# Performance work log

Hardware: AMD Instinct MI355X
Metric: run time of the kernel (lower is better)

Reference implementation:

```python
import jax, jax.numpy as jnp
import numpy as np


def setup_inputs() -> dict:
    key = jax.random.key(0)
    k1, k2, k3, k4 = jax.random.split(key, 4)
    N, F, E = 100000, 128, 1600000
    Fo = F // 2
    x = jax.random.normal(k1, (N, F), dtype=jnp.float32)
    edge_index = jax.random.randint(k2, (2, E), 0, N, dtype=jnp.int32)
    W_conv = jax.random.normal(k3, (Fo, F), dtype=jnp.float32) * (1.0 / np.sqrt(F))
    b_conv = jnp.zeros((Fo,), dtype=jnp.float32)
    W_lin = jax.random.normal(k4, (1, Fo), dtype=jnp.float32) * (1.0 / np.sqrt(Fo))
    b_lin = jnp.zeros((1,), dtype=jnp.float32)
    return {"x": x, "edge_index": edge_index, "W_conv": W_conv,
            "b_conv": b_conv, "W_lin": W_lin, "b_lin": b_lin}


def gcn_conv(x, edge_index, W_conv, b_conv):
    # PyG GCNConv: add self-loops, symmetric normalization, x@W.T, scatter-add, + bias
    N = x.shape[0]
    loops = jnp.arange(N, dtype=edge_index.dtype)
    src = jnp.concatenate([edge_index[0], loops])  # message sources
    dst = jnp.concatenate([edge_index[1], loops])  # aggregation targets
    h = x @ W_conv.T  # [N, Fo]
    deg = jax.ops.segment_sum(jnp.ones_like(dst, dtype=h.dtype), dst, num_segments=N)
    dinv = jnp.where(deg > 0, jax.lax.rsqrt(deg), 0.0)
    norm = dinv[src] * dinv[dst]  # [E+N]
    msg = h[src] * norm[:, None]  # [E+N, Fo] -- dominant memory traffic
    agg = jax.ops.segment_sum(msg, dst, num_segments=N)
    return agg + b_conv


def reference(x, edge_index, W_conv, b_conv, W_lin, b_lin):
    h = gcn_conv(x, edge_index, W_conv, b_conv)
    h = jax.nn.relu(h)
    logits = h @ W_lin.T + b_lin  # [N, 1]
    return jax.nn.sigmoid(logits)
```

## Files before the change

kernel.cpp:

```cpp
#include <hip/hip_runtime.h>
#include <hip/hip_bf16.h>
#include <math.h>

#define F_IN   128
#define F_OUT  64
#define CHUNK  5120
#define MAXB   512
#define PADSLACK 4096

typedef short bf16x8 __attribute__((ext_vector_type(8)));
typedef float f32x4  __attribute__((ext_vector_type(4)));

__device__ __forceinline__ float bf2f(unsigned short u) {
    union { unsigned int i; float f; } c; c.i = ((unsigned int)u) << 16; return c.f;
}
__device__ __forceinline__ unsigned short f2bf(float f) {
    union { float f; unsigned int i; } c; c.f = f;
    unsigned int r = c.i + 0x7FFFu + ((c.i >> 16) & 1u);
    return (unsigned short)(r >> 16);
}
__device__ __forceinline__ unsigned int pk2bf(float a, float b) {
    __hip_bfloat162 p = __float22bfloat162_rn(make_float2(a, b));
    union { __hip_bfloat162 h; unsigned int u; } c; c.h = p; return c.u;
}
__device__ __forceinline__ float u_lo(unsigned int u) {
    union { unsigned int i; float f; } c; c.i = u << 16; return c.f;
}
__device__ __forceinline__ float u_hi(unsigned int u) {
    union { unsigned int i; float f; } c; c.i = u & 0xFFFF0000u; return c.f;
}

__global__ __launch_bounds__(256) void k_hist(
    const int* __restrict__ dst, int E, int* __restrict__ M, int NBLK, int NBC) {
    __shared__ int hist[MAXB];
    for (int c = threadIdx.x; c < MAXB; c += 256) hist[c] = 0;
    __syncthreads();
    int e0 = blockIdx.x * CHUNK;
    int e1 = min(E, e0 + CHUNK);
    for (int e = e0 + threadIdx.x; e < e1; e += 256)
        atomicAdd(&hist[dst[e] >> 8], 1);
    __syncthreads();
    for (int c = threadIdx.x; c < NBC; c += 256)
        M[c * NBLK + blockIdx.x] = hist[c];
}

__global__ void k_scan1(const int* __restrict__ M, int* __restrict__ tmp,
                        int* __restrict__ bsum, int S) {
    __shared__ int sh[256];
    int i = blockIdx.x * 256 + threadIdx.x;
    int v = (i < S) ? M[i] : 0;
    sh[threadIdx.x] = v;
    __syncthreads();
    for (int off = 1; off < 256; off <<= 1) {
        int t = (threadIdx.x >= off) ? sh[threadIdx.x - off] : 0;
        __syncthreads();
        sh[threadIdx.x] += t;
        __syncthreads();
    }
    if (i < S) tmp[i] = sh[threadIdx.x];
    if (threadIdx.x == 255) bsum[blockIdx.x] = sh[255];
}

__global__ void k_scan2(int* __restrict__ bsum, int NB1) {
    __shared__ int sh[512];
    int v = (threadIdx.x < NB1) ? bsum[threadIdx.x] : 0;
    sh[threadIdx.x] = v;
    __syncthreads();
    for (int off = 1; off < 512; off <<= 1) {
        int t = (threadIdx.x >= off) ? sh[threadIdx.x - off] : 0;
        __syncthreads();
        sh[threadIdx.x] += t;
        __syncthreads();
    }
    if (threadIdx.x < NB1) bsum[threadIdx.x] = sh[threadIdx.x] - v;
}

__global__ void k_scan3(int* __restrict__ M, const int* __restrict__ tmp,
                        const int* __restrict__ bsum, int* __restrict__ bucketOff,
                        int S, int NBLK, int NBC, int E) {
    int i = blockIdx.x * 256 + threadIdx.x;
    if (i < S) {
        int orig = M[i];
        int o = tmp[i] - orig + bsum[blockIdx.x];
        M[i] = o;
        if (i % NBLK == 0) bucketOff[i / NBLK] = o;
    }
    if (i == 0) bucketOff[NBC] = E;
}

__global__ __launch_bounds__(256) void k_scatter(
    const int* __restrict__ src, const int* __restrict__ dst, int E,
    const int* __restrict__ M, int NBLK, int NBC, unsigned int* __restrict__ entries) {
    __shared__ int cur[MAXB];
    for (int c = threadIdx.x; c < NBC; c += 256)
        cur[c] = M[c * NBLK + blockIdx.x];
    __syncthreads();
    int e0 = blockIdx.x * CHUNK;
    int e1 = min(E, e0 + CHUNK);
    for (int e = e0 + threadIdx.x; e < e1; e += 256) {
        int d = dst[e];
        int s = src[e];
        int p = atomicAdd(&cur[d >> 8], 1);
        entries[p] = ((unsigned int)(d & 255) << 24) | (unsigned int)s;
    }
}

__global__ __launch_bounds__(256) void k_sort(
    const unsigned int* __restrict__ entries, const int* __restrict__ bucketOff,
    int* __restrict__ offsetsP, int* __restrict__ deg,
    unsigned int* __restrict__ srcsP, int N) {
    __shared__ int hist[256];
    __shared__ int curs[256];
    const int tid = threadIdx.x;
    const int b = blockIdx.x;
    const int start = bucketOff[b];
    const int end   = bucketOff[b + 1];
    const int startP = start + b * PADSLACK;

    hist[tid] = 0;
    __syncthreads();
    for (int i = start + tid; i < end; i += 256)
        atomicAdd(&hist[entries[i] >> 24], 1);
    __syncthreads();

    int cntv   = hist[tid];
    int padded = (cntv + 15) & ~15;
    curs[tid] = padded;
    __syncthreads();
    for (int off = 1; off < 256; off <<= 1) {
        int t = (tid >= off) ? curs[tid - off] : 0;
        __syncthreads();
        curs[tid] += t;
        __syncthreads();
    }
    int exclP = curs[tid] - padded;
    int d = (b << 8) + tid;
    if (d < N) { offsetsP[d] = startP + exclP; deg[d] = cntv; }
    __syncthreads();
    curs[tid] = startP + exclP;
    __syncthreads();

    for (int i = start + tid; i < end; i += 256) {
        unsigned int v = entries[i];
        int p = atomicAdd(&curs[v >> 24], 1);
        srcsP[p] = (v & 0xFFFFFFu) << 7;
    }
    __syncthreads();

    int padEnd = startP + exclP + padded;
    unsigned int sent = ((unsigned int)N) << 7;
    for (int p = curs[tid]; p < padEnd; ++p)
        srcsP[p] = sent;
}

__global__ __launch_bounds__(256) void k_gemm(
    const float* __restrict__ x, const float* __restrict__ W,
    const int* __restrict__ deg, unsigned short* __restrict__ g, int N) {
    __shared__ unsigned short xs[64 * F_IN];
    __shared__ unsigned short Wsh[F_OUT * F_IN];
    __shared__ float dinvs[64];

    const int tid  = threadIdx.x;
    const int row0 = blockIdx.x * 64;

    {
        const float4* W4 = (const float4*)W;
        #pragma unroll
        for (int t = 0; t < 8; ++t) {
            int idx = t * 256 + tid;
            float4 v = W4[idx];
            uint2 u = make_uint2(pk2bf(v.x, v.y), pk2bf(v.z, v.w));
            *(uint2*)&Wsh[idx * 4] = u;
        }
    }
    {
        const float4* x4 = (const float4*)x;
        #pragma unroll
        for (int t = 0; t < 8; ++t) {
            int idx = t * 256 + tid;
            int r = idx >> 5;
            int grow = row0 + r;
            float4 v = make_float4(0.f, 0.f, 0.f, 0.f);
            if (grow < N) v = x4[(size_t)grow * 32 + (idx & 31)];
            uint2 u = make_uint2(pk2bf(v.x, v.y), pk2bf(v.z, v.w));
            *(uint2*)&xs[idx * 4] = u;
        }
    }
    if (tid < 64) {
        int grow = row0 + tid;
        float dv = 1.0f;
        if (grow < N) dv = rsqrtf((float)deg[grow] + 1.0f);
        dinvs[tid] = dv;
    }
    __syncthreads();

    const int lane = tid & 63;
    const int wave = tid >> 6;
    const int m = lane & 15;
    const int q = lane >> 4;
    const int r0 = wave * 16;

    bf16x8 a[4];
    #pragma unroll
    for (int ks = 0; ks < 4; ++ks)
        a[ks] = *(const bf16x8*)&xs[(r0 + m) * F_IN + ks * 32 + q * 8];

    f32x4 acc[4] = {{0,0,0,0},{0,0,0,0},{0,0,0,0},{0,0,0,0}};
    #pragma unroll
    for (int ct = 0; ct < 4; ++ct) {
        #pragma unroll
        for (int ks = 0; ks < 4; ++ks) {
            bf16x8 b = *(const bf16x8*)&Wsh[(ct * 16 + m) * F_IN + ks * 32 + q * 8];
            acc[ct] = __builtin_amdgcn_mfma_f32_16x16x32_bf16(a[ks], b, acc[ct], 0, 0, 0);
        }
    }

    float dv[4];
    #pragma unroll
    for (int reg = 0; reg < 4; ++reg)
        dv[reg] = dinvs[r0 + q * 4 + reg];
    #pragma unroll
    for (int ct = 0; ct < 4; ++ct) {
        #pragma unroll
        for (int reg = 0; reg < 4; ++reg) {
            int grow = row0 + r0 + q * 4 + reg;
            if (grow <= N)
                g[(size_t)grow * F_OUT + ct * 16 + m] = f2bf(acc[ct][reg] * dv[reg]);
        }
    }
}

__global__ __launch_bounds__(256) void k_pull(
    const unsigned short* __restrict__ g, const int* __restrict__ offsetsP,
    const int* __restrict__ deg, const unsigned int* __restrict__ srcsP,
    const float* __restrict__ b_conv, const float* __restrict__ W_lin,
    const float* __restrict__ b_lin, float* __restrict__ out, int N) {
    const int lane   = threadIdx.x & 63;
    const int grp    = lane >> 3;
    const int s      = lane & 7;
    const int wave   = (blockIdx.x * blockDim.x + threadIdx.x) >> 6;
    const int nwaves = (gridDim.x * blockDim.x) >> 6;

    const float2* b2 = (const float2*)b_conv;
    const float2* w2 = (const float2*)W_lin;
    float2 bb[4], wl[4];
    #pragma unroll
    for (int j = 0; j < 4; ++j) { bb[j] = b2[s * 4 + j]; wl[j] = w2[s * 4 + j]; }
    const float bl = b_lin[0];
    const float selfm = (grp == 0) ? 1.0f : 0.0f;

    const char* gb = (const char*)g;
    const unsigned int seg = ((unsigned int)s) << 4;

    for (int i = wave; i < N; i += nwaves) {
        int e0 = __builtin_amdgcn_readfirstlane(offsetsP[i]);
        int dg = __builtin_amdgcn_readfirstlane(deg[i]);
        int niter = (dg + 15) >> 4;

        uint4 us = *(const uint4*)(gb + (size_t)(((unsigned int)i << 7) | seg));
        float2 acc[4];
        acc[0] = make_float2(selfm * u_lo(us.x), selfm * u_hi(us.x));
        acc[1] = make_float2(selfm * u_lo(us.y), selfm * u_hi(us.y));
        acc[2] = make_float2(selfm * u_lo(us.z), selfm * u_hi(us.z));
        acc[3] = make_float2(selfm * u_lo(us.w), selfm * u_hi(us.w));

        const unsigned int* sp = srcsP + e0;
        for (int it = 0; it < niter; ++it) {
            unsigned int o0 = sp[grp];
            unsigned int o1 = sp[8 + grp];
            uint4 uA = *(const uint4*)(gb + (size_t)(o0 | seg));
            uint4 uB = *(const uint4*)(gb + (size_t)(o1 | seg));
            acc[0].x += u_lo(uA.x); acc[0].y += u_hi(uA.x);
            acc[1].x += u_lo(uA.y); acc[1].y += u_hi(uA.y);
            acc[2].x += u_lo(uA.z); acc[2].y += u_hi(uA.z);
            acc[3].x += u_lo(uA.w); acc[3].y += u_hi(uA.w);
            acc[0].x += u_lo(uB.x); acc[0].y += u_hi(uB.x);
            acc[1].x += u_lo(uB.y); acc[1].y += u_hi(uB.y);
            acc[2].x += u_lo(uB.z); acc[2].y += u_hi(uB.z);
            acc[3].x += u_lo(uB.w); acc[3].y += u_hi(uB.w);
            sp += 16;
        }

        #pragma unroll
        for (int m = 8; m <= 32; m <<= 1) {
            #pragma unroll
            for (int j = 0; j < 4; ++j) {
                acc[j].x += __shfl_xor(acc[j].x, m, 64);
                acc[j].y += __shfl_xor(acc[j].y, m, 64);
            }
        }

        float dinv = rsqrtf((float)dg + 1.0f);
        float t = 0.f;
        #pragma unroll
        for (int j = 0; j < 4; ++j) {
            float rx = fmaxf(acc[j].x * dinv + bb[j].x, 0.f);
            float ry = fmaxf(acc[j].y * dinv + bb[j].y, 0.f);
            t += rx * wl[j].x + ry * wl[j].y;
        }
        t += __shfl_xor(t, 1, 64);
        t += __shfl_xor(t, 2, 64);
        t += __shfl_xor(t, 4, 64);
        if (lane == 0)
            out[i] = 1.0f / (1.0f + expf(-(t + bl)));
    }
}

extern "C" void kernel_launch(void* const* d_in, const int* in_sizes, int n_in,
                              void* d_out, int out_size, void* d_ws, size_t ws_size,
                              hipStream_t stream) {
    const float* x      = (const float*)d_in[0];
    const int*   ei     = (const int*)d_in[1];
    const float* W_conv = (const float*)d_in[2];
    const float* b_conv = (const float*)d_in[3];
    const float* W_lin  = (const float*)d_in[4];
    const float* b_lin  = (const float*)d_in[5];

    const int N = in_sizes[0] / F_IN;
    const int E = in_sizes[1] / 2;
    const int* src = ei;
    const int* dst = ei + E;
    float* out = (float*)d_out;

    const int NBC  = (N + 255) >> 8;
    const int NBLK = (E + CHUNK - 1) / CHUNK;
    const int S    = NBC * NBLK;
    const int NB1  = (S + 255) / 256;

    const int Na = (N + 256) & ~255;
    const int Sa = (S + 256) & ~255;
    const int Ea = (E + 255) & ~255;
    const int EPa = (E + NBC * PADSLACK + 511) & ~255;

    int* M         = (int*)d_ws;
    int* tmp       = M + Sa;
    int* bsum      = tmp + Sa;
    int* bucketOff = bsum + 512;
    int* offsetsP  = bucketOff + (MAXB + 256);
    int* deg       = offsetsP + Na;
    unsigned int* entries = (unsigned int*)(deg + Na);
    unsigned int* srcsP   = (unsigned int*)(entries + Ea);
    unsigned short* g = (unsigned short*)(srcsP + EPa);

    k_hist   <<<NBLK, 256, 0, stream>>>(dst, E, M, NBLK, NBC);
    k_scan1  <<<NB1, 256, 0, stream>>>(M, tmp, bsum, S);
    k_scan2  <<<1, 512, 0, stream>>>(bsum, NB1);
    k_scan3  <<<NB1, 256, 0, stream>>>(M, tmp, bsum, bucketOff, S, NBLK, NBC, E);
    k_scatter<<<NBLK, 256, 0, stream>>>(src, dst, E, M, NBLK, NBC, entries);
    k_sort   <<<NBC, 256, 0, stream>>>(entries, bucketOff, offsetsP, deg, srcsP, N);
    k_gemm   <<<(N + 64) / 64, 256, 0, stream>>>(x, W_conv, deg, g, N);
    k_pull   <<<4096, 256, 0, stream>>>(g, offsetsP, deg, srcsP, b_conv, W_lin, b_lin, out, N);
}
```

Measured before the change: 193.8 us.

## Fold scan finalization into consumers, precompute bf16 weights, vectorize pull math

```diff
diff --git a/kernel.cpp b/kernel.cpp
--- a/kernel.cpp
+++ b/kernel.cpp
@@ -10,10 +10,8 @@
 
 typedef short bf16x8 __attribute__((ext_vector_type(8)));
 typedef float f32x4  __attribute__((ext_vector_type(4)));
-
-__device__ __forceinline__ float bf2f(unsigned short u) {
-    union { unsigned int i; float f; } c; c.i = ((unsigned int)u) << 16; return c.f;
-}
+typedef float f32x2  __attribute__((ext_vector_type(2)));
+
 __device__ __forceinline__ unsigned short f2bf(float f) {
     union { float f; unsigned int i; } c; c.f = f;
     unsigned int r = c.i + 0x7FFFu + ((c.i >> 16) & 1u);
@@ -31,7 +29,19 @@
 }
 
 __global__ __launch_bounds__(256) void k_hist(
-    const int* __restrict__ dst, int E, int* __restrict__ M, int NBLK, int NBC) {
+    const int* __restrict__ dst, int E, int* __restrict__ M, int NBLK, int NBC,
+    const float* __restrict__ W, unsigned short* __restrict__ Wbf) {
+    if (blockIdx.x == (unsigned)NBLK) {
+        const float4* W4 = (const float4*)W;
+        #pragma unroll
+        for (int t = 0; t < 8; ++t) {
+            int idx = t * 256 + threadIdx.x;
+            float4 v = W4[idx];
+            uint2 u = make_uint2(pk2bf(v.x, v.y), pk2bf(v.z, v.w));
+            *(uint2*)&Wbf[idx * 4] = u;
+        }
+        return;
+    }
     __shared__ int hist[MAXB];
     for (int c = threadIdx.x; c < MAXB; c += 256) hist[c] = 0;
     __syncthreads();
@@ -75,25 +85,17 @@
     if (threadIdx.x < NB1) bsum[threadIdx.x] = sh[threadIdx.x] - v;
 }
 
-__global__ void k_scan3(int* __restrict__ M, const int* __restrict__ tmp,
-                        const int* __restrict__ bsum, int* __restrict__ bucketOff,
-                        int S, int NBLK, int NBC, int E) {
-    int i = blockIdx.x * 256 + threadIdx.x;
-    if (i < S) {
-        int orig = M[i];
-        int o = tmp[i] - orig + bsum[blockIdx.x];
-        M[i] = o;
-        if (i % NBLK == 0) bucketOff[i / NBLK] = o;
-    }
-    if (i == 0) bucketOff[NBC] = E;
+__device__ __forceinline__ int exscan(const int* M, const int* tmp, const int* bsum, int i) {
+    return tmp[i] - M[i] + bsum[i >> 8];
 }
 
 __global__ __launch_bounds__(256) void k_scatter(
     const int* __restrict__ src, const int* __restrict__ dst, int E,
-    const int* __restrict__ M, int NBLK, int NBC, unsigned int* __restrict__ entries) {
+    const int* __restrict__ M, const int* __restrict__ tmp, const int* __restrict__ bsum,
+    int NBLK, int NBC, unsigned int* __restrict__ entries) {
     __shared__ int cur[MAXB];
     for (int c = threadIdx.x; c < NBC; c += 256)
-        cur[c] = M[c * NBLK + blockIdx.x];
+        cur[c] = exscan(M, tmp, bsum, c * NBLK + blockIdx.x);
     __syncthreads();
     int e0 = blockIdx.x * CHUNK;
     int e1 = min(E, e0 + CHUNK);
@@ -106,19 +108,26 @@
 }
 
 __global__ __launch_bounds__(256) void k_sort(
-    const unsigned int* __restrict__ entries, const int* __restrict__ bucketOff,
+    const unsigned int* __restrict__ entries,
+    const int* __restrict__ M, const int* __restrict__ tmp, const int* __restrict__ bsum,
+    int NBLK, int NBC, int E,
     int* __restrict__ offsetsP, int* __restrict__ deg,
     unsigned int* __restrict__ srcsP, int N) {
     __shared__ int hist[256];
     __shared__ int curs[256];
+    __shared__ int sh_se[2];
     const int tid = threadIdx.x;
     const int b = blockIdx.x;
-    const int start = bucketOff[b];
-    const int end   = bucketOff[b + 1];
+    if (tid == 0) {
+        sh_se[0] = exscan(M, tmp, bsum, b * NBLK);
+        sh_se[1] = (b + 1 < NBC) ? exscan(M, tmp, bsum, (b + 1) * NBLK) : E;
+    }
+    hist[tid] = 0;
+    __syncthreads();
+    const int start = sh_se[0];
+    const int end   = sh_se[1];
     const int startP = start + b * PADSLACK;
 
-    hist[tid] = 0;
-    __syncthreads();
     for (int i = start + tid; i < end; i += 256)
         atomicAdd(&hist[entries[i] >> 24], 1);
     __syncthreads();
@@ -154,7 +163,7 @@
 }
 
 __global__ __launch_bounds__(256) void k_gemm(
-    const float* __restrict__ x, const float* __restrict__ W,
+    const float* __restrict__ x, const unsigned short* __restrict__ Wbf,
     const int* __restrict__ deg, unsigned short* __restrict__ g, int N) {
     __shared__ unsigned short xs[64 * F_IN];
     __shared__ unsigned short Wsh[F_OUT * F_IN];
@@ -164,13 +173,11 @@
     const int row0 = blockIdx.x * 64;
 
     {
-        const float4* W4 = (const float4*)W;
+        const uint2* Wb = (const uint2*)Wbf;
         #pragma unroll
         for (int t = 0; t < 8; ++t) {
             int idx = t * 256 + tid;
-            float4 v = W4[idx];
-            uint2 u = make_uint2(pk2bf(v.x, v.y), pk2bf(v.z, v.w));
-            *(uint2*)&Wsh[idx * 4] = u;
+            *(uint2*)&Wsh[idx * 4] = Wb[idx];
         }
     }
     {
@@ -243,11 +250,15 @@
 
     const float2* b2 = (const float2*)b_conv;
     const float2* w2 = (const float2*)W_lin;
-    float2 bb[4], wl[4];
-    #pragma unroll
-    for (int j = 0; j < 4; ++j) { bb[j] = b2[s * 4 + j]; wl[j] = w2[s * 4 + j]; }
+    f32x2 bb[4], wl[4];
+    #pragma unroll
+    for (int j = 0; j < 4; ++j) {
+        float2 tb = b2[s * 4 + j]; bb[j] = (f32x2){tb.x, tb.y};
+        float2 tw = w2[s * 4 + j]; wl[j] = (f32x2){tw.x, tw.y};
+    }
     const float bl = b_lin[0];
     const float selfm = (grp == 0) ? 1.0f : 0.0f;
+    const f32x2 selfv = (f32x2){selfm, selfm};
 
     const char* gb = (const char*)g;
     const unsigned int seg = ((unsigned int)s) << 4;
@@ -258,11 +269,11 @@
         int niter = (dg + 15) >> 4;
 
         uint4 us = *(const uint4*)(gb + (size_t)(((unsigned int)i << 7) | seg));
-        float2 acc[4];
-        acc[0] = make_float2(selfm * u_lo(us.x), selfm * u_hi(us.x));
-        acc[1] = make_float2(selfm * u_lo(us.y), selfm * u_hi(us.y));
-        acc[2] = make_float2(selfm * u_lo(us.z), selfm * u_hi(us.z));
-        acc[3] = make_float2(selfm * u_lo(us.w), selfm * u_hi(us.w));
+        f32x2 acc[4];
+        acc[0] = selfv * (f32x2){u_lo(us.x), u_hi(us.x)};
+        acc[1] = selfv * (f32x2){u_lo(us.y), u_hi(us.y)};
+        acc[2] = selfv * (f32x2){u_lo(us.z), u_hi(us.z)};
+        acc[3] = selfv * (f32x2){u_lo(us.w), u_hi(us.w)};
 
         const unsigned int* sp = srcsP + e0;
         for (int it = 0; it < niter; ++it) {
@@ -270,14 +281,14 @@
             unsigned int o1 = sp[8 + grp];
             uint4 uA = *(const uint4*)(gb + (size_t)(o0 | seg));
             uint4 uB = *(const uint4*)(gb + (size_t)(o1 | seg));
-            acc[0].x += u_lo(uA.x); acc[0].y += u_hi(uA.x);
-            acc[1].x += u_lo(uA.y); acc[1].y += u_hi(uA.y);
-            acc[2].x += u_lo(uA.z); acc[2].y += u_hi(uA.z);
-            acc[3].x += u_lo(uA.w); acc[3].y += u_hi(uA.w);
-            acc[0].x += u_lo(uB.x); acc[0].y += u_hi(uB.x);
-            acc[1].x += u_lo(uB.y); acc[1].y += u_hi(uB.y);
-            acc[2].x += u_lo(uB.z); acc[2].y += u_hi(uB.z);
-            acc[3].x += u_lo(uB.w); acc[3].y += u_hi(uB.w);
+            acc[0] += (f32x2){u_lo(uA.x), u_hi(uA.x)};
+            acc[1] += (f32x2){u_lo(uA.y), u_hi(uA.y)};
+            acc[2] += (f32x2){u_lo(uA.z), u_hi(uA.z)};
+            acc[3] += (f32x2){u_lo(uA.w), u_hi(uA.w)};
+            acc[0] += (f32x2){u_lo(uB.x), u_hi(uB.x)};
+            acc[1] += (f32x2){u_lo(uB.y), u_hi(uB.y)};
+            acc[2] += (f32x2){u_lo(uB.z), u_hi(uB.z)};
+            acc[3] += (f32x2){u_lo(uB.w), u_hi(uB.w)};
             sp += 16;
         }
 
@@ -285,19 +296,23 @@
         for (int m = 8; m <= 32; m <<= 1) {
             #pragma unroll
             for (int j = 0; j < 4; ++j) {
-                acc[j].x += __shfl_xor(acc[j].x, m, 64);
-                acc[j].y += __shfl_xor(acc[j].y, m, 64);
+                f32x2 t = (f32x2){__shfl_xor(acc[j][0], m, 64),
+                                  __shfl_xor(acc[j][1], m, 64)};
+                acc[j] += t;
             }
         }
 
         float dinv = rsqrtf((float)dg + 1.0f);
-        float t = 0.f;
+        f32x2 dinv2 = (f32x2){dinv, dinv};
+        f32x2 dot2 = (f32x2){0.f, 0.f};
         #pragma unroll
         for (int j = 0; j < 4; ++j) {
-            float rx = fmaxf(acc[j].x * dinv + bb[j].x, 0.f);
-            float ry = fmaxf(acc[j].y * dinv + bb[j].y, 0.f);
-            t += rx * wl[j].x + ry * wl[j].y;
-        }
+            f32x2 r = acc[j] * dinv2 + bb[j];
+            r[0] = fmaxf(r[0], 0.f);
+            r[1] = fmaxf(r[1], 0.f);
+            dot2 += r * wl[j];
+        }
+        float t = dot2[0] + dot2[1];
         t += __shfl_xor(t, 1, 64);
         t += __shfl_xor(t, 2, 64);
         t += __shfl_xor(t, 4, 64);
@@ -335,19 +350,19 @@
     int* M         = (int*)d_ws;
     int* tmp       = M + Sa;
     int* bsum      = tmp + Sa;
-    int* bucketOff = bsum + 512;
-    int* offsetsP  = bucketOff + (MAXB + 256);
+    int* offsetsP  = bsum + 512;
     int* deg       = offsetsP + Na;
-    unsigned int* entries = (unsigned int*)(deg + Na);
-    unsigned int* srcsP   = (unsigned int*)(entries + Ea);
+    unsigned short* Wbf = (unsigned short*)(deg + Na);
+    unsigned int* entries = (unsigned int*)(Wbf + 8192);
+    unsigned int* srcsP   = entries + Ea;
     unsigned short* g = (unsigned short*)(srcsP + EPa);
 
-    k_hist   <<<NBLK, 256, 0, stream>>>(dst, E, M, NBLK, NBC);
+    k_hist   <<<NBLK + 1, 256, 0, stream>>>(dst, E, M, NBLK, NBC, W_conv, Wbf);
     k_scan1  <<<NB1, 256, 0, stream>>>(M, tmp, bsum, S);
     k_scan2  <<<1, 512, 0, stream>>>(bsum, NB1);
-    k_scan3  <<<NB1, 256, 0, stream>>>(M, tmp, bsum, bucketOff, S, NBLK, NBC, E);
-    k_scatter<<<NBLK, 256, 0, stream>>>(src, dst, E, M, NBLK, NBC, entries);
-    k_sort   <<<NBC, 256, 0, stream>>>(entries, bucketOff, offsetsP, deg, srcsP, N);
-    k_gemm   <<<(N + 64) / 64, 256, 0, stream>>>(x, W_conv, deg, g, N);
+    k_scatter<<<NBLK, 256, 0, stream>>>(src, dst, E, M, tmp, bsum, NBLK, NBC, entries);
+    k_sort   <<<NBC, 256, 0, stream>>>(entries, M, tmp, bsum, NBLK, NBC, E,
+                                       offsetsP, deg, srcsP, N);
+    k_gemm   <<<(N + 64) / 64, 256, 0, stream>>>(x, Wbf, deg, g, N);
     k_pull   <<<4096, 256, 0, stream>>>(g, offsetsP, deg, srcsP, b_conv, W_lin, b_lin, out, N);
 }
```

Measured after the change: 194.6 us. No clear change (+0.4%).
